# Optimization experiments

Hardware: AMD Instinct MI355X
Metric: run time of the kernel (lower is better)

The kernel has to match this reference:

```python
import jax, jax.numpy as jnp
import numpy as np

EMBED_DIM = 256
NUM_HEADS = 8
HEAD_DIM = EMBED_DIM // NUM_HEADS
SCALING = HEAD_DIM ** 0.5  # NOTE: module MULTIPLIES q by sqrt(head_dim), faithful to source


def setup_inputs() -> dict:
    key = jax.random.key(0)
    ks = jax.random.split(key, 10)
    B, S, D = 8, 1024, EMBED_DIM
    w = lambda k: jax.random.normal(k, (D, D), dtype=jnp.float32) * (1.0 / np.sqrt(D))
    b = lambda k: jax.random.normal(k, (D,), dtype=jnp.float32) * 0.01
    return {
        "hidden_states": jax.random.normal(ks[0], (B, S, D), dtype=jnp.float32),
        "object_queries": jax.random.normal(ks[1], (B, S, D), dtype=jnp.float32),
        "Wq": w(ks[2]), "bq": b(ks[3]),
        "Wk": w(ks[4]), "bk": b(ks[5]),
        "Wv": w(ks[6]), "bv": b(ks[7]),
        "Wo": w(ks[8]), "bo": b(ks[9]),
    }


def reference(hidden_states, object_queries, Wq, bq, Wk, bk, Wv, bv, Wo, bo):
    B, S, D = hidden_states.shape
    hs_pos = hidden_states + object_queries  # with_pos_embed for q and k
    # nn.Linear: x @ W.T + b (W is [out, in])
    q = (hs_pos @ Wq.T + bq) * SCALING
    k = hs_pos @ Wk.T + bk
    v = hidden_states @ Wv.T + bv  # value uses original hidden states (no pos)
    # [B, S, H, Dh]
    q = q.reshape(B, S, NUM_HEADS, HEAD_DIM)
    k = k.reshape(B, S, NUM_HEADS, HEAD_DIM)
    v = v.reshape(B, S, NUM_HEADS, HEAD_DIM)
    scores = jnp.einsum("bqhd,bkhd->bhqk", q, k)  # [B, H, S, S]
    probs = jax.nn.softmax(scores, axis=-1)
    out = jnp.einsum("bhqk,bkhd->bqhd", probs, v).reshape(B, S, D)
    return out @ Wo.T + bo
```

## Files before the change

### kernel.cpp

```cpp
#include <hip/hip_runtime.h>
#include <math.h>

#define BATCH 8
#define SEQ 1024
#define DM 256
#define NH 8
#define DH 32
#define MTOT (BATCH*SEQ)
#define LOG2E 1.4426950408889634f
#define SCALING 5.656854249492381f
#define QSCALE (SCALING * LOG2E)

typedef __attribute__((ext_vector_type(8))) short short8;
typedef __attribute__((ext_vector_type(4))) float f32x4;
typedef __attribute__((ext_vector_type(4))) unsigned short us4;
typedef _Float16 f16;
typedef __attribute__((ext_vector_type(8))) _Float16 f16x8;
typedef __attribute__((ext_vector_type(4))) _Float16 f16x4;

__device__ inline unsigned short f2bf(float f){
  union { float f; unsigned u; } x; x.f = f;
  unsigned r = x.u + 0x7fffu + ((x.u >> 16) & 1u);
  return (unsigned short)(r >> 16);
}
__device__ inline float bf2f(unsigned short s){
  union { unsigned u; float f; } x; x.u = ((unsigned)s) << 16;
  return x.f;
}
__device__ inline float fast_exp2(float x){
  float r; asm("v_exp_f32 %0, %1" : "=v"(r) : "v"(x)); return r;
}

__device__ inline f32x4 mfma_bf16(short8 a, short8 b, f32x4 c){
  return __builtin_amdgcn_mfma_f32_16x16x32_bf16(a, b, c, 0, 0, 0);
}
__device__ inline f32x4 mfma_f16_32(f16x8 a, f16x8 b, f32x4 c){
  return __builtin_amdgcn_mfma_f32_16x16x32_f16(a, b, c, 0, 0, 0);
}
__device__ inline f32x4 mfma_f16_16(f16x4 a, f16x4 b, f32x4 c){
  return __builtin_amdgcn_mfma_f32_16x16x16f16(a, b, c, 0, 0, 0);
}

__global__ __launch_bounds__(256) void prep_x_kernel(
    const float* __restrict__ hs, const float* __restrict__ oq,
    unsigned short* __restrict__ xph, unsigned short* __restrict__ xpl,
    f16* __restrict__ xv){
  const int n4 = MTOT * DM / 4;
  for (int i = blockIdx.x * blockDim.x + threadIdx.x; i < n4;
       i += gridDim.x * blockDim.x){
    f32x4 h = ((const f32x4*)hs)[i];
    f32x4 q = ((const f32x4*)oq)[i];
    us4 ph, pl; f16x4 xv4;
#pragma unroll
    for (int j = 0; j < 4; ++j){
      float p = h[j] + q[j];
      unsigned short hi = f2bf(p);
      ph[j] = hi;
      pl[j] = f2bf(p - bf2f(hi));
      xv4[j] = (f16)h[j];
    }
    ((us4*)xph)[i] = ph;
    ((us4*)xpl)[i] = pl;
    ((f16x4*)xv)[i] = xv4;
  }
}

__global__ __launch_bounds__(256) void prep_w_kernel(
    const float* __restrict__ Wq, const float* __restrict__ Wk,
    const float* __restrict__ Wv, const float* __restrict__ Wo,
    unsigned short* __restrict__ wqh, unsigned short* __restrict__ wql,
    unsigned short* __restrict__ wkh, unsigned short* __restrict__ wkl,
    f16* __restrict__ wv16, f16* __restrict__ wo16){
  int i = blockIdx.x * blockDim.x + threadIdx.x;
  if (i < DM * DM){
    float q = Wq[i];
    unsigned short qh_ = f2bf(q);
    wqh[i] = qh_; wql[i] = f2bf(q - bf2f(qh_));
    float k = Wk[i];
    unsigned short kh_ = f2bf(k);
    wkh[i] = kh_; wkl[i] = f2bf(k - bf2f(kh_));
    wv16[i] = (f16)Wv[i];
    wo16[i] = (f16)Wo[i];
  }
}

__global__ __launch_bounds__(256, 2) void proj_qkv_kernel(
    const unsigned short* __restrict__ xph, const unsigned short* __restrict__ xpl,
    const f16* __restrict__ xv,
    const unsigned short* __restrict__ wqh, const unsigned short* __restrict__ wql,
    const unsigned short* __restrict__ wkh, const unsigned short* __restrict__ wkl,
    const f16* __restrict__ wv16,
    const float* __restrict__ bq, const float* __restrict__ bk, const float* __restrict__ bv,
    unsigned short* __restrict__ qhp, unsigned short* __restrict__ qlp,
    unsigned short* __restrict__ khp, unsigned short* __restrict__ klp,
    f16* __restrict__ vout){
  __shared__ unsigned short XH[128][40];
  __shared__ unsigned short XL[128][40];
  __shared__ f16 XV[128][40];
  __shared__ unsigned short WQH[64][40];
  __shared__ unsigned short WQL[64][40];
  __shared__ unsigned short WKH[64][40];
  __shared__ unsigned short WKL[64][40];
  __shared__ f16 WV[64][40];
  const int tid = threadIdx.x;
  const int lane = tid & 63, wave = tid >> 6;
  const int bid = blockIdx.x;
  const int xcd = bid & 7, g = bid >> 3;
  const int nb = g & 3, mb = xcd * 8 + (g >> 2);
  const int m0 = mb * 128, n0 = nb * 64;
  const int wm = wave >> 1, wn = wave & 1;
  const int r = lane & 15, jj = lane >> 4;

  const int sr = tid >> 2, ssl = (tid & 3) * 8;
  const size_t xo0 = (size_t)(m0 + sr) * DM + ssl;
  const size_t xo1 = (size_t)(m0 + sr + 64) * DM + ssl;
  const size_t wo = (size_t)(n0 + sr) * DM + ssl;

  short8 rxh0, rxh1, rxl0, rxl1, rwq, rwql_, rwk, rwkl_;
  f16x8 rxv0, rxv1, rwv;
  rxh0 = *(const short8*)(xph + xo0); rxh1 = *(const short8*)(xph + xo1);
  rxl0 = *(const short8*)(xpl + xo0); rxl1 = *(const short8*)(xpl + xo1);
  rxv0 = *(const f16x8*)(xv + xo0);   rxv1 = *(const f16x8*)(xv + xo1);
  rwq = *(const short8*)(wqh + wo);   rwql_ = *(const short8*)(wql + wo);
  rwk = *(const short8*)(wkh + wo);   rwkl_ = *(const short8*)(wkl + wo);
  rwv = *(const f16x8*)(wv16 + wo);

  f32x4 aq[4][2], ak[4][2], av[4][2];
#pragma unroll
  for (int mi = 0; mi < 4; ++mi)
#pragma unroll
    for (int ni = 0; ni < 2; ++ni){
      aq[mi][ni] = (f32x4){0.f,0.f,0.f,0.f};
      ak[mi][ni] = (f32x4){0.f,0.f,0.f,0.f};
      av[mi][ni] = (f32x4){0.f,0.f,0.f,0.f};
    }

  for (int kk = 0; kk < DM; kk += 32){
    __syncthreads();
    *(short8*)&XH[sr][ssl] = rxh0;  *(short8*)&XH[sr + 64][ssl] = rxh1;
    *(short8*)&XL[sr][ssl] = rxl0;  *(short8*)&XL[sr + 64][ssl] = rxl1;
    *(f16x8*)&XV[sr][ssl] = rxv0;   *(f16x8*)&XV[sr + 64][ssl] = rxv1;
    *(short8*)&WQH[sr][ssl] = rwq;  *(short8*)&WQL[sr][ssl] = rwql_;
    *(short8*)&WKH[sr][ssl] = rwk;  *(short8*)&WKL[sr][ssl] = rwkl_;
    *(f16x8*)&WV[sr][ssl] = rwv;
    __syncthreads();
    if (kk + 32 < DM){
      const int o = kk + 32;
      rxh0 = *(const short8*)(xph + xo0 + o); rxh1 = *(const short8*)(xph + xo1 + o);
      rxl0 = *(const short8*)(xpl + xo0 + o); rxl1 = *(const short8*)(xpl + xo1 + o);
      rxv0 = *(const f16x8*)(xv + xo0 + o);   rxv1 = *(const f16x8*)(xv + xo1 + o);
      rwq = *(const short8*)(wqh + wo + o);   rwql_ = *(const short8*)(wql + wo + o);
      rwk = *(const short8*)(wkh + wo + o);   rwkl_ = *(const short8*)(wkl + wo + o);
      rwv = *(const f16x8*)(wv16 + wo + o);
    }
#pragma unroll
    for (int ni = 0; ni < 2; ++ni){
      const int brow = wn * 32 + ni * 16 + r;
      short8 bwqh = *(const short8*)&WQH[brow][jj * 8];
      short8 bwql = *(const short8*)&WQL[brow][jj * 8];
      short8 bwkh = *(const short8*)&WKH[brow][jj * 8];
      short8 bwkl = *(const short8*)&WKL[brow][jj * 8];
      f16x8 bwv = *(const f16x8*)&WV[brow][jj * 8];
#pragma unroll
      for (int mi = 0; mi < 4; ++mi){
        const int arow = wm * 64 + mi * 16 + r;
        short8 axh = *(const short8*)&XH[arow][jj * 8];
        short8 axl = *(const short8*)&XL[arow][jj * 8];
        f16x8 axv = *(const f16x8*)&XV[arow][jj * 8];
        aq[mi][ni] = mfma_bf16(axh, bwqh, aq[mi][ni]);
        aq[mi][ni] = mfma_bf16(axh, bwql, aq[mi][ni]);
        aq[mi][ni] = mfma_bf16(axl, bwqh, aq[mi][ni]);
        ak[mi][ni] = mfma_bf16(axh, bwkh, ak[mi][ni]);
        ak[mi][ni] = mfma_bf16(axh, bwkl, ak[mi][ni]);
        ak[mi][ni] = mfma_bf16(axl, bwkh, ak[mi][ni]);
        av[mi][ni] = mfma_f16_32(axv, bwv, av[mi][ni]);
      }
    }
  }
#pragma unroll
  for (int ni = 0; ni < 2; ++ni){
    const int col = n0 + wn * 32 + ni * 16 + r;
    const float bqc = bq[col] * QSCALE;
    const float bkc = bk[col];
    const float bvc = bv[col];
#pragma unroll
    for (int mi = 0; mi < 4; ++mi){
#pragma unroll
      for (int rr = 0; rr < 4; ++rr){
        const int row = m0 + wm * 64 + mi * 16 + jj * 4 + rr;
        float qv = aq[mi][ni][rr] * QSCALE + bqc;
        unsigned short qhi = f2bf(qv);
        qhp[row * DM + col] = qhi;
        qlp[row * DM + col] = f2bf(qv - bf2f(qhi));
        float kv = ak[mi][ni][rr] + bkc;
        unsigned short khi = f2bf(kv);
        khp[row * DM + col] = khi;
        klp[row * DM + col] = f2bf(kv - bf2f(khi));
        vout[row * DM + col] = (f16)(av[mi][ni][rr] + bvc);
      }
    }
  }
}

__global__ __launch_bounds__(256) void transpose_v_kernel(
    const f16* __restrict__ v, f16* __restrict__ vT){
  __shared__ unsigned short tile[64][65];
  const int b = blockIdx.z;
  const int s0 = blockIdx.x * 64;
  const int c0 = blockIdx.y * 64;
  const int t = threadIdx.x;
  const int r = t >> 2;
  const int cc = (t & 3) * 16;
  const unsigned short* src =
      (const unsigned short*)v + ((size_t)(b * SEQ + s0 + r)) * DM + c0 + cc;
  short8 a0 = *(const short8*)(src);
  short8 a1 = *(const short8*)(src + 8);
#pragma unroll
  for (int j = 0; j < 8; ++j){
    tile[r][cc + j] = (unsigned short)a0[j];
    tile[r][cc + 8 + j] = (unsigned short)a1[j];
  }
  __syncthreads();
  short8 o0, o1;
#pragma unroll
  for (int j = 0; j < 8; ++j){
    o0[j] = (short)tile[cc + j][r];
    o1[j] = (short)tile[cc + 8 + j][r];
  }
  unsigned short* dst =
      (unsigned short*)vT + ((size_t)(b * DM + c0 + r)) * SEQ + s0 + cc;
  *(short8*)(dst) = o0;
  *(short8*)(dst + 8) = o1;
}

__global__ __launch_bounds__(256) void attn_kernel(
    const unsigned short* __restrict__ qh, const unsigned short* __restrict__ ql,
    const unsigned short* __restrict__ kh, const unsigned short* __restrict__ kl,
    const f16* __restrict__ vT, f16* __restrict__ aout){
  __shared__ unsigned short KH[2][64][40];
  __shared__ unsigned short KL[2][64][40];
  __shared__ f16 VT[2][32][72];
  const int lane = threadIdx.x & 63;
  const int wave = threadIdx.x >> 6;
  const int tid = threadIdx.x;
  const int bh = blockIdx.x >> 3;
  const int b = bh >> 3, h = bh & 7;
  const int q0 = ((blockIdx.x & 7) * 4 + wave) * 32;
  const int rowbase = b * SEQ;
  const int col0 = h * DH;
  const int r = lane & 15, jj = lane >> 4;

  const int qrowA = rowbase + q0 + r;
  const int qrowB = qrowA + 16;
  short8 bqhA = *(const short8*)(qh + qrowA * DM + col0 + jj * 8);
  short8 bqlA = *(const short8*)(ql + qrowA * DM + col0 + jj * 8);
  short8 bqhB = *(const short8*)(qh + qrowB * DM + col0 + jj * 8);
  short8 bqlB = *(const short8*)(ql + qrowB * DM + col0 + jj * 8);

  const int skey = tid >> 2, ssl = tid & 3;
  const unsigned short* khsrc = kh + (size_t)(rowbase + skey) * DM + col0 + ssl * 8;
  const unsigned short* klsrc = kl + (size_t)(rowbase + skey) * DM + col0 + ssl * 8;
  const int sdh = tid >> 3, ss8 = tid & 7;
  const f16* vsrc = vT + (size_t)(b * DM + col0 + sdh) * SEQ + ss8 * 8;

  short8 rkh = *(const short8*)(khsrc);
  short8 rkl = *(const short8*)(klsrc);
  f16x8 rv = *(const f16x8*)(vsrc);

  float mA = -INFINITY, lsumA = 0.f;
  float mB = -INFINITY, lsumB = 0.f;
  f32x4 o0a = {0.f,0.f,0.f,0.f}, o1a = {0.f,0.f,0.f,0.f};
  f32x4 o0b = {0.f,0.f,0.f,0.f}, o1b = {0.f,0.f,0.f,0.f};

  for (int c = 0; c < SEQ; c += 64){
    const int p = (c >> 6) & 1;
    *(short8*)&KH[p][skey][ssl * 8] = rkh;
    *(short8*)&KL[p][skey][ssl * 8] = rkl;
    *(f16x8*)&VT[p][sdh][ss8 * 8] = rv;
    __syncthreads();
    if (c + 64 < SEQ){
      rkh = *(const short8*)(khsrc + (size_t)(c + 64) * DM);
      rkl = *(const short8*)(klsrc + (size_t)(c + 64) * DM);
      rv = *(const f16x8*)(vsrc + c + 64);
    }
    f32x4 sA[4], sB[4];
    float cmaxA = -INFINITY, cmaxB = -INFINITY;
#pragma unroll
    for (int t = 0; t < 4; ++t){
      short8 akh = *(const short8*)&KH[p][t * 16 + r][jj * 8];
      short8 akl = *(const short8*)&KL[p][t * 16 + r][jj * 8];
      f32x4 sv = {0.f,0.f,0.f,0.f};
      sv = mfma_bf16(akh, bqhA, sv);
      sv = mfma_bf16(akh, bqlA, sv);
      sv = mfma_bf16(akl, bqhA, sv);
      sA[t] = sv;
      cmaxA = fmaxf(cmaxA, fmaxf(fmaxf(sv[0], sv[1]), fmaxf(sv[2], sv[3])));
      f32x4 sw = {0.f,0.f,0.f,0.f};
      sw = mfma_bf16(akh, bqhB, sw);
      sw = mfma_bf16(akh, bqlB, sw);
      sw = mfma_bf16(akl, bqhB, sw);
      sB[t] = sw;
      cmaxB = fmaxf(cmaxB, fmaxf(fmaxf(sw[0], sw[1]), fmaxf(sw[2], sw[3])));
    }
    cmaxA = fmaxf(cmaxA, __shfl_xor(cmaxA, 16, 64));
    cmaxA = fmaxf(cmaxA, __shfl_xor(cmaxA, 32, 64));
    cmaxB = fmaxf(cmaxB, __shfl_xor(cmaxB, 16, 64));
    cmaxB = fmaxf(cmaxB, __shfl_xor(cmaxB, 32, 64));
    if (!__all(cmaxA - mA <= 8.0f)){
      const float mnew = fmaxf(mA, cmaxA);
      const float scale = fast_exp2(mA - mnew);
      lsumA *= scale;
#pragma unroll
      for (int rr = 0; rr < 4; ++rr){ o0a[rr] *= scale; o1a[rr] *= scale; }
      mA = mnew;
    }
    if (!__all(cmaxB - mB <= 8.0f)){
      const float mnew = fmaxf(mB, cmaxB);
      const float scale = fast_exp2(mB - mnew);
      lsumB *= scale;
#pragma unroll
      for (int rr = 0; rr < 4; ++rr){ o0b[rr] *= scale; o1b[rr] *= scale; }
      mB = mnew;
    }
    float psA = 0.f, psB = 0.f;
    f16x4 bpA[4], bpB[4];
#pragma unroll
    for (int t = 0; t < 4; ++t){
      float a0 = fast_exp2(sA[t][0] - mA);
      float a1 = fast_exp2(sA[t][1] - mA);
      float a2 = fast_exp2(sA[t][2] - mA);
      float a3 = fast_exp2(sA[t][3] - mA);
      psA += (a0 + a1) + (a2 + a3);
      f16x4 ba; ba[0]=(f16)a0; ba[1]=(f16)a1; ba[2]=(f16)a2; ba[3]=(f16)a3;
      bpA[t] = ba;
      float b0 = fast_exp2(sB[t][0] - mB);
      float b1 = fast_exp2(sB[t][1] - mB);
      float b2 = fast_exp2(sB[t][2] - mB);
      float b3 = fast_exp2(sB[t][3] - mB);
      psB += (b0 + b1) + (b2 + b3);
      f16x4 bb; bb[0]=(f16)b0; bb[1]=(f16)b1; bb[2]=(f16)b2; bb[3]=(f16)b3;
      bpB[t] = bb;
    }
    psA += __shfl_xor(psA, 16, 64);
    psA += __shfl_xor(psA, 32, 64);
    lsumA += psA;
    psB += __shfl_xor(psB, 16, 64);
    psB += __shfl_xor(psB, 32, 64);
    lsumB += psB;
#pragma unroll
    for (int t = 0; t < 4; ++t){
      f16x4 av0 = *(const f16x4*)&VT[p][r][t * 16 + jj * 4];
      f16x4 av1 = *(const f16x4*)&VT[p][16 + r][t * 16 + jj * 4];
      o0a = mfma_f16_16(av0, bpA[t], o0a);
      o1a = mfma_f16_16(av1, bpA[t], o1a);
      o0b = mfma_f16_16(av0, bpB[t], o0b);
      o1b = mfma_f16_16(av1, bpB[t], o1b);
    }
  }
  const float invA = 1.f / lsumA;
  const float invB = 1.f / lsumB;
  const int orowA = qrowA * DM + col0;
  const int orowB = qrowB * DM + col0;
#pragma unroll
  for (int rr = 0; rr < 4; ++rr){
    const int dh = jj * 4 + rr;
    aout[orowA + dh] = (f16)(o0a[rr] * invA);
    aout[orowA + 16 + dh] = (f16)(o1a[rr] * invA);
    aout[orowB + dh] = (f16)(o0b[rr] * invB);
    aout[orowB + 16 + dh] = (f16)(o1b[rr] * invB);
  }
}

__global__ __launch_bounds__(256, 4) void oproj_kernel(
    const f16* __restrict__ attn, const f16* __restrict__ wo16,
    const float* __restrict__ bo, float* __restrict__ out){
  __shared__ f16 AT[128][40];
  __shared__ f16 WO[64][40];
  const int tid = threadIdx.x;
  const int lane = tid & 63, wave = tid >> 6;
  const int bid = blockIdx.x;
  const int xcd = bid & 7, g = bid >> 3;
  const int nb = g & 3, mb = xcd * 8 + (g >> 2);
  const int m0 = mb * 128, n0 = nb * 64;
  const int wm = wave >> 1, wn = wave & 1;
  const int r = lane & 15, jj = lane >> 4;
  const int sr = tid >> 2, ssl = (tid & 3) * 8;
  const f16* asrc0 = attn + (size_t)(m0 + sr) * DM + ssl;
  const f16* asrc1 = attn + (size_t)(m0 + sr + 64) * DM + ssl;
  const f16* wsrc = wo16 + (size_t)(n0 + sr) * DM + ssl;
  f16x8 ra0 = *(const f16x8*)(asrc0);
  f16x8 ra1 = *(const f16x8*)(asrc1);
  f16x8 rw = *(const f16x8*)(wsrc);
  f32x4 acc[4][2];
#pragma unroll
  for (int mi = 0; mi < 4; ++mi){
    acc[mi][0] = (f32x4){0.f,0.f,0.f,0.f};
    acc[mi][1] = (f32x4){0.f,0.f,0.f,0.f};
  }
  for (int kk = 0; kk < DM; kk += 32){
    __syncthreads();
    *(f16x8*)&AT[sr][ssl] = ra0;
    *(f16x8*)&AT[sr + 64][ssl] = ra1;
    *(f16x8*)&WO[sr][ssl] = rw;
    __syncthreads();
    if (kk + 32 < DM){
      ra0 = *(const f16x8*)(asrc0 + kk + 32);
      ra1 = *(const f16x8*)(asrc1 + kk + 32);
      rw = *(const f16x8*)(wsrc + kk + 32);
    }
    f16x8 bf0 = *(const f16x8*)&WO[wn * 32 + r][jj * 8];
    f16x8 bf1 = *(const f16x8*)&WO[wn * 32 + 16 + r][jj * 8];
#pragma unroll
    for (int mi = 0; mi < 4; ++mi){
      f16x8 af = *(const f16x8*)&AT[wm * 64 + mi * 16 + r][jj * 8];
      acc[mi][0] = mfma_f16_32(af, bf0, acc[mi][0]);
      acc[mi][1] = mfma_f16_32(af, bf1, acc[mi][1]);
    }
  }
#pragma unroll
  for (int ni = 0; ni < 2; ++ni){
    const int col = n0 + wn * 32 + ni * 16 + r;
    const float bc = bo[col];
#pragma unroll
    for (int mi = 0; mi < 4; ++mi){
#pragma unroll
      for (int rr = 0; rr < 4; ++rr){
        const int row = m0 + wm * 64 + mi * 16 + jj * 4 + rr;
        out[row * DM + col] = acc[mi][ni][rr] + bc;
      }
    }
  }
}

extern "C" void kernel_launch(void* const* d_in, const int* in_sizes, int n_in,
                              void* d_out, int out_size, void* d_ws, size_t ws_size,
                              hipStream_t stream){
  const float* hs = (const float*)d_in[0];
  const float* oq = (const float*)d_in[1];
  const float* Wq = (const float*)d_in[2];
  const float* bq = (const float*)d_in[3];
  const float* Wk = (const float*)d_in[4];
  const float* bk = (const float*)d_in[5];
  const float* Wv = (const float*)d_in[6];
  const float* bv = (const float*)d_in[7];
  const float* Wo = (const float*)d_in[8];
  const float* bo = (const float*)d_in[9];
  float* out = (float*)d_out;

  char* p = (char*)d_ws;
  auto alloc = [&](size_t bytes) -> char* {
    char* r = p;
    p += (bytes + 255) & ~((size_t)255);
    return r;
  };
  const size_t xb = (size_t)MTOT * DM * 2;
  unsigned short* xph = (unsigned short*)alloc(xb);
  unsigned short* xpl = (unsigned short*)alloc(xb);
  f16* xv = (f16*)alloc(xb);
  unsigned short* qh = (unsigned short*)alloc(xb);
  unsigned short* ql = (unsigned short*)alloc(xb);
  unsigned short* kh = (unsigned short*)alloc(xb);
  unsigned short* kl = (unsigned short*)alloc(xb);
  f16* vv = (f16*)alloc(xb);
  f16* attn = (f16*)alloc(xb);
  const size_t wb = (size_t)DM * DM * 2;
  unsigned short* wqh = (unsigned short*)alloc(wb);
  unsigned short* wql = (unsigned short*)alloc(wb);
  unsigned short* wkh = (unsigned short*)alloc(wb);
  unsigned short* wkl = (unsigned short*)alloc(wb);
  f16* wv16 = (f16*)alloc(wb);
  f16* wo16 = (f16*)alloc(wb);
  f16* vT = (f16*)xph;

  hipLaunchKernelGGL(prep_x_kernel, dim3(1024), dim3(256), 0, stream,
                     hs, oq, xph, xpl, xv);
  hipLaunchKernelGGL(prep_w_kernel, dim3(DM * DM / 256), dim3(256), 0, stream,
                     Wq, Wk, Wv, Wo, wqh, wql, wkh, wkl, wv16, wo16);
  hipLaunchKernelGGL(proj_qkv_kernel, dim3(256), dim3(256), 0, stream,
                     xph, xpl, xv, wqh, wql, wkh, wkl, wv16, bq, bk, bv,
                     qh, ql, kh, kl, vv);
  hipLaunchKernelGGL(transpose_v_kernel, dim3(16, 4, 8), dim3(256), 0, stream,
                     vv, vT);
  hipLaunchKernelGGL(attn_kernel, dim3(512), dim3(256), 0, stream,
                     qh, ql, kh, kl, vT, attn);
  hipLaunchKernelGGL(oproj_kernel, dim3(256), dim3(256), 0, stream,
                     attn, wo16, bo, out);
}
```

Baseline: 75.04 us.

## Fuse V transpose into QKV projection epilogue and remap attention blocks per XCD

The projection kernel now writes V already transposed, staging it through an extra shared-memory tile, so the separate transpose_v kernel and its global round trip go away. The attention kernel's block index is also remapped so that all query blocks of a batch-head pair land on the same XCD, which should improve L2 reuse of K and V. The extra 18KB of LDS in the projection kernel may reduce its occupancy below the requested two blocks per CU.

```diff
diff --git a/kernel.cpp b/kernel.cpp
--- a/kernel.cpp
+++ b/kernel.cpp
@@ -93,7 +93,7 @@
     const float* __restrict__ bq, const float* __restrict__ bk, const float* __restrict__ bv,
     unsigned short* __restrict__ qhp, unsigned short* __restrict__ qlp,
     unsigned short* __restrict__ khp, unsigned short* __restrict__ klp,
-    f16* __restrict__ vout){
+    f16* __restrict__ vT){
   __shared__ unsigned short XH[128][40];
   __shared__ unsigned short XL[128][40];
   __shared__ f16 XV[128][40];
@@ -102,6 +102,7 @@
   __shared__ unsigned short WKH[64][40];
   __shared__ unsigned short WKL[64][40];
   __shared__ f16 WV[64][40];
+  __shared__ f16 VTT[64][144];
   const int tid = threadIdx.x;
   const int lane = tid & 63, wave = tid >> 6;
   const int bid = blockIdx.x;
@@ -185,6 +186,7 @@
     const float bvc = bv[col];
 #pragma unroll
     for (int mi = 0; mi < 4; ++mi){
+      f16x4 v4;
 #pragma unroll
       for (int rr = 0; rr < 4; ++rr){
         const int row = m0 + wm * 64 + mi * 16 + jj * 4 + rr;
@@ -196,41 +198,20 @@
         unsigned short khi = f2bf(kv);
         khp[row * DM + col] = khi;
         klp[row * DM + col] = f2bf(kv - bf2f(khi));
-        vout[row * DM + col] = (f16)(av[mi][ni][rr] + bvc);
+        v4[rr] = (f16)(av[mi][ni][rr] + bvc);
       }
-    }
-  }
-}
-
-__global__ __launch_bounds__(256) void transpose_v_kernel(
-    const f16* __restrict__ v, f16* __restrict__ vT){
-  __shared__ unsigned short tile[64][65];
-  const int b = blockIdx.z;
-  const int s0 = blockIdx.x * 64;
-  const int c0 = blockIdx.y * 64;
-  const int t = threadIdx.x;
-  const int r = t >> 2;
-  const int cc = (t & 3) * 16;
-  const unsigned short* src =
-      (const unsigned short*)v + ((size_t)(b * SEQ + s0 + r)) * DM + c0 + cc;
-  short8 a0 = *(const short8*)(src);
-  short8 a1 = *(const short8*)(src + 8);
-#pragma unroll
-  for (int j = 0; j < 8; ++j){
-    tile[r][cc + j] = (unsigned short)a0[j];
-    tile[r][cc + 8 + j] = (unsigned short)a1[j];
+      *(f16x4*)&VTT[wn * 32 + ni * 16 + r][wm * 64 + mi * 16 + jj * 4] = v4;
+    }
   }
   __syncthreads();
-  short8 o0, o1;
-#pragma unroll
-  for (int j = 0; j < 8; ++j){
-    o0[j] = (short)tile[cc + j][r];
-    o1[j] = (short)tile[cc + 8 + j][r];
-  }
-  unsigned short* dst =
-      (unsigned short*)vT + ((size_t)(b * DM + c0 + r)) * SEQ + s0 + cc;
-  *(short8*)(dst) = o0;
-  *(short8*)(dst + 8) = o1;
+  const int batch = m0 >> 10;
+  const int s0 = m0 & 1023;
+  const int c = tid >> 2, sblk = (tid & 3) * 32;
+  f16* dst = vT + ((size_t)(batch * DM + n0 + c)) * SEQ + s0 + sblk;
+#pragma unroll
+  for (int u = 0; u < 4; ++u){
+    *(f16x8*)(dst + u * 8) = *(const f16x8*)&VTT[c][sblk + u * 8];
+  }
 }
 
 __global__ __launch_bounds__(256) void attn_kernel(
@@ -243,9 +224,11 @@
   const int lane = threadIdx.x & 63;
   const int wave = threadIdx.x >> 6;
   const int tid = threadIdx.x;
-  const int bh = blockIdx.x >> 3;
+  const int xcd = blockIdx.x & 7, j = blockIdx.x >> 3;
+  const int bh = xcd * 8 + (j & 7);
+  const int qb = j >> 3;
   const int b = bh >> 3, h = bh & 7;
-  const int q0 = ((blockIdx.x & 7) * 4 + wave) * 32;
+  const int q0 = (qb * 4 + wave) * 32;
   const int rowbase = b * SEQ;
   const int col0 = h * DH;
   const int r = lane & 15, jj = lane >> 4;
@@ -461,7 +444,7 @@
   unsigned short* ql = (unsigned short*)alloc(xb);
   unsigned short* kh = (unsigned short*)alloc(xb);
   unsigned short* kl = (unsigned short*)alloc(xb);
-  f16* vv = (f16*)alloc(xb);
+  f16* vT = (f16*)alloc(xb);
   f16* attn = (f16*)alloc(xb);
   const size_t wb = (size_t)DM * DM * 2;
   unsigned short* wqh = (unsigned short*)alloc(wb);
@@ -470,7 +453,6 @@
   unsigned short* wkl = (unsigned short*)alloc(wb);
   f16* wv16 = (f16*)alloc(wb);
   f16* wo16 = (f16*)alloc(wb);
-  f16* vT = (f16*)xph;
 
   hipLaunchKernelGGL(prep_x_kernel, dim3(1024), dim3(256), 0, stream,
                      hs, oq, xph, xpl, xv);
@@ -478,9 +460,7 @@
                      Wq, Wk, Wv, Wo, wqh, wql, wkh, wkl, wv16, wo16);
   hipLaunchKernelGGL(proj_qkv_kernel, dim3(256), dim3(256), 0, stream,
                      xph, xpl, xv, wqh, wql, wkh, wkl, wv16, bq, bk, bv,
-                     qh, ql, kh, kl, vv);
-  hipLaunchKernelGGL(transpose_v_kernel, dim3(16, 4, 8), dim3(256), 0, stream,
-                     vv, vT);
+                     qh, ql, kh, kl, vT);
   hipLaunchKernelGGL(attn_kernel, dim3(512), dim3(256), 0, stream,
                      qh, ql, kh, kl, vT, attn);
   hipLaunchKernelGGL(oproj_kernel, dim3(256), dim3(256), 0, stream,
```

After: 69.20 us. 1.08x faster.
